# Kernel optimization log

Measured on AMD Instinct MI355X. Metric: run time of the kernel, lower is better.

## Reference

```python
import jax, jax.numpy as jnp
import numpy as np

BINS = 10


def _neg_pearson(p, t):
    # global standardization (torch.std default is unbiased, ddof=1)
    p = (p - p.mean()) / p.std(ddof=1)
    t = (t - t.mean()) / t.std(ddof=1)
    N = p.shape[1]
    sx = p.sum(1); sy = t.sum(1)
    sxy = (p * t).sum(1)
    sx2 = (p * p).sum(1); sy2 = (t * t).sum(1)
    pear = (N * sxy - sx * sy) / jnp.sqrt((N * sx2 - sx**2) * (N * sy2 - sy**2))
    return (1.0 - pear).mean()


def _hann(N):
    # torch.hann_window is periodic: 0.5*(1 - cos(2*pi*n/N))
    return 0.5 * (1.0 - jnp.cos(2.0 * jnp.pi * jnp.arange(N, dtype=jnp.float32) / N))


def _phase_correlation(x, t):
    # torch.stft with n_fft=seq_len, center=False, hann window -> single frame = rfft(x*hann)
    N = x.shape[1]
    w = _hann(N)
    xf = jnp.fft.rfft(x * w, axis=1)   # [B, N//2+1]
    tf = jnp.fft.rfft(t * w, axis=1)
    corr = xf * jnp.conj(tf)
    corr = corr / jnp.abs(corr)        # phase-only correlation
    cm = jnp.fft.irfft(corr, n=N, axis=1)  # [B, N]
    idx = jnp.argmax(cm, axis=1)
    return 1.0 - jnp.mean(jnp.cos(2.0 * jnp.pi * idx / N))


def _power_spectrum(x, t):
    xp = jnp.abs(jnp.fft.rfft(x, axis=1)) ** 2
    tp = jnp.abs(jnp.fft.rfft(t, axis=1)) ** 2
    return jnp.mean(jnp.abs(xp - tp)) / jnp.mean(tp)


def _mutual_information(x, y, bins=BINS):
    B, S = x.shape
    xmin = x.min(1); xmax = x.max(1)
    ymin = y.min(1); ymax = y.max(1)
    bwx = (xmax - xmin) / bins
    bwy = (ymax - ymin) / bins
    ix = jnp.clip(((x - xmin[:, None]) / bwx[:, None]).astype(jnp.int32), 0, bins - 1)
    iy = jnp.clip(((y - ymin[:, None]) / bwy[:, None]).astype(jnp.int32), 0, bins - 1)
    flat = ix * bins + iy  # [B, S]
    # vectorized 2D histogram via scatter-add (replaces the python double loop)
    hist = jax.vmap(lambda f: jnp.zeros(bins * bins, jnp.float32).at[f].add(1.0))(flat)
    hist = hist.reshape(B, bins, bins)
    hx = hist.sum(2); hy = hist.sum(1)
    denom = B * S  # NOTE: original normalizes by batch*seq (faithful reproduction)
    px = hx / denom; py = hy / denom; pxy = hist / denom
    eps = 1e-8
    mi = (pxy * jnp.log((pxy + eps) / (px[:, :, None] * py[:, None, :] + eps))).sum((1, 2))
    hxe = -(px * jnp.log(px + eps)).sum(1)
    hye = -(py * jnp.log(py + eps)).sum(1)
    nmi = mi / ((hxe + hye) / 2.0)
    return 1.0 - nmi.mean()


def setup_inputs() -> dict:
    key = jax.random.key(0)
    k1, k2 = jax.random.split(key)
    return {
        "predictions": jax.random.normal(k1, (2, 512, 16384), dtype=jnp.float32),
        "targets": jax.random.normal(k2, (512, 16384), dtype=jnp.float32),
        "i": 0,
        "epoch": 700,
    }


def reference(predictions, targets, i, epoch):
    p = predictions[i]  # [B, S]
    loss = _neg_pearson(p, targets)
    if epoch >= 400:
        loss = loss + _phase_correlation(p, targets)
        loss = loss + _power_spectrum(p, targets)
    if epoch >= 700:
        loss = loss + _mutual_information(p, targets)
    return loss
```

## Files before the change

kernel.cpp:

```cpp
#include <hip/hip_runtime.h>
#include <math.h>

#define BB 512
#define SS 16384
#define TPIF 6.28318530717958647692f

#define PD(i) ((i) + ((i) >> 4) + ((i) >> 8))
#define NPD 17472
#define BBASE 8200

__device__ __forceinline__ int sp(int k) {
    int s = ((k & 7) << 11) + (((k >> 3) & 7) << 8) + (((k >> 6) & 7) << 5)
          + (((k >> 9) & 7) << 2) + ((k >> 12) & 3);
    return PD(s);
}


template <int SGN, int LOG2Q>
__device__ __forceinline__ void stage_dif8(float2* sz, int t) {
    constexpr int Q = 1 << LOG2Q;
    constexpr int DQ = Q + (Q >> 4) + (Q >> 8);
    const float sg = (float)SGN;
    const float r2 = 0.70710678118654752f;
    #pragma unroll 1
    for (int c = 0; c < 2; ++c) {
        const int j = t + (c << 10);
        const int g = j >> LOG2Q;
        const int p = j & (Q - 1);
        const int i0 = PD((g << (LOG2Q + 3)) + p);
        int idx[8];
        #pragma unroll
        for (int k = 0; k < 8; ++k)
            idx[k] = (LOG2Q >= 4) ? (i0 + k * DQ) : (i0 + 4 * k + (k >> 2));
        float2 z[8];
        #pragma unroll
        for (int k = 0; k < 8; ++k) z[k] = sz[idx[k]];
        float2 a0, a1, a2, a3, b0, b1, b2, b3;
        a0 = make_float2(z[0].x + z[4].x, z[0].y + z[4].y);
        b0 = make_float2(z[0].x - z[4].x, z[0].y - z[4].y);
        a1 = make_float2(z[1].x + z[5].x, z[1].y + z[5].y);
        b1 = make_float2(z[1].x - z[5].x, z[1].y - z[5].y);
        a2 = make_float2(z[2].x + z[6].x, z[2].y + z[6].y);
        b2 = make_float2(z[2].x - z[6].x, z[2].y - z[6].y);
        a3 = make_float2(z[3].x + z[7].x, z[3].y + z[7].y);
        b3 = make_float2(z[3].x - z[7].x, z[3].y - z[7].y);
        { float x = b1.x, y = b1.y; b1 = make_float2(r2 * (x - sg * y), r2 * (y + sg * x)); }
        { float x = b2.x, y = b2.y; b2 = make_float2(-sg * y, sg * x); }
        { float x = b3.x, y = b3.y; b3 = make_float2(-r2 * (x + sg * y), r2 * (sg * x - y)); }
        float2 o[8];
        {
            float t0r = a0.x + a2.x, t0i = a0.y + a2.y;
            float t1r = a0.x - a2.x, t1i = a0.y - a2.y;
            float t2r = a1.x + a3.x, t2i = a1.y + a3.y;
            float t3r = a1.x - a3.x, t3i = a1.y - a3.y;
            o[0] = make_float2(t0r + t2r, t0i + t2i);
            o[4] = make_float2(t0r - t2r, t0i - t2i);
            o[2] = make_float2(t1r - sg * t3i, t1i + sg * t3r);
            o[6] = make_float2(t1r + sg * t3i, t1i - sg * t3r);
        }
        {
            float t0r = b0.x + b2.x, t0i = b0.y + b2.y;
            float t1r = b0.x - b2.x, t1i = b0.y - b2.y;
            float t2r = b1.x + b3.x, t2i = b1.y + b3.y;
            float t3r = b1.x - b3.x, t3i = b1.y - b3.y;
            o[1] = make_float2(t0r + t2r, t0i + t2i);
            o[5] = make_float2(t0r - t2r, t0i - t2i);
            o[3] = make_float2(t1r - sg * t3i, t1i + sg * t3r);
            o[7] = make_float2(t1r + sg * t3i, t1i - sg * t3r);
        }
        const float arev = sg * (float)p * (1.0f / (8.0f * (float)Q));
        const float cb = __builtin_amdgcn_cosf(arev);
        const float sb = __builtin_amdgcn_sinf(arev);
        sz[idx[0]] = o[0];
        float wr = cb, wi = sb;
        #pragma unroll
        for (int r = 1; r < 8; ++r) {
            sz[idx[r]] = make_float2(o[r].x * wr - o[r].y * wi,
                                     o[r].x * wi + o[r].y * wr);
            float nr = wr * cb - wi * sb, ni = wr * sb + wi * cb;
            wr = nr; wi = ni;
        }
    }
    __syncthreads();
}

template <int SGN>
__device__ __forceinline__ void stage_nt4(float2* sz, int t) {
    const float sg = (float)SGN;
    #pragma unroll 1
    for (int c = 0; c < 4; ++c) {
        const int j = t + (c << 10);
        const int i0 = 4 * j + (j >> 2) + (j >> 6);
        float2 z0 = sz[i0], z1 = sz[i0 + 1], z2 = sz[i0 + 2], z3 = sz[i0 + 3];
        float t0r = z0.x + z2.x, t0i = z0.y + z2.y;
        float t1r = z0.x - z2.x, t1i = z0.y - z2.y;
        float t2r = z1.x + z3.x, t2i = z1.y + z3.y;
        float t3r = z1.x - z3.x, t3i = z1.y - z3.y;
        sz[i0]     = make_float2(t0r + t2r, t0i + t2i);
        sz[i0 + 2] = make_float2(t0r - t2r, t0i - t2i);
        sz[i0 + 1] = make_float2(t1r - sg * t3i, t1i + sg * t3r);
        sz[i0 + 3] = make_float2(t1r + sg * t3i, t1i - sg * t3r);
    }
    __syncthreads();
}

template <int SGN, int LOG2Q>
__device__ __forceinline__ void stage8k_dif8(float2* bz, int t) {
    constexpr int Q = 1 << LOG2Q;
    constexpr int DQ = Q + (Q >> 4) + (Q >> 8);
    constexpr int CORR = (LOG2Q == 7) ? 1 : 0;
    const float sg = (float)SGN;
    const float r2 = 0.70710678118654752f;
    const int g = t >> LOG2Q;
    const int p = t & (Q - 1);
    const int i0 = PD((g << (LOG2Q + 3)) + p);
    int idx[8];
    #pragma unroll
    for (int k = 0; k < 8; ++k) idx[k] = i0 + k * DQ + CORR * (k >> 1);
    float2 z[8];
    #pragma unroll
    for (int k = 0; k < 8; ++k) z[k] = bz[idx[k]];
    float2 a0, a1, a2, a3, b0, b1, b2, b3;
    a0 = make_float2(z[0].x + z[4].x, z[0].y + z[4].y);
    b0 = make_float2(z[0].x - z[4].x, z[0].y - z[4].y);
    a1 = make_float2(z[1].x + z[5].x, z[1].y + z[5].y);
    b1 = make_float2(z[1].x - z[5].x, z[1].y - z[5].y);
    a2 = make_float2(z[2].x + z[6].x, z[2].y + z[6].y);
    b2 = make_float2(z[2].x - z[6].x, z[2].y - z[6].y);
    a3 = make_float2(z[3].x + z[7].x, z[3].y + z[7].y);
    b3 = make_float2(z[3].x - z[7].x, z[3].y - z[7].y);
    { float x = b1.x, y = b1.y; b1 = make_float2(r2 * (x - sg * y), r2 * (y + sg * x)); }
    { float x = b2.x, y = b2.y; b2 = make_float2(-sg * y, sg * x); }
    { float x = b3.x, y = b3.y; b3 = make_float2(-r2 * (x + sg * y), r2 * (sg * x - y)); }
    float2 o[8];
    {
        float t0r = a0.x + a2.x, t0i = a0.y + a2.y;
        float t1r = a0.x - a2.x, t1i = a0.y - a2.y;
        float t2r = a1.x + a3.x, t2i = a1.y + a3.y;
        float t3r = a1.x - a3.x, t3i = a1.y - a3.y;
        o[0] = make_float2(t0r + t2r, t0i + t2i);
        o[4] = make_float2(t0r - t2r, t0i - t2i);
        o[2] = make_float2(t1r - sg * t3i, t1i + sg * t3r);
        o[6] = make_float2(t1r + sg * t3i, t1i - sg * t3r);
    }
    {
        float t0r = b0.x + b2.x, t0i = b0.y + b2.y;
        float t1r = b0.x - b2.x, t1i = b0.y - b2.y;
        float t2r = b1.x + b3.x, t2i = b1.y + b3.y;
        float t3r = b1.x - b3.x, t3i = b1.y - b3.y;
        o[1] = make_float2(t0r + t2r, t0i + t2i);
        o[5] = make_float2(t0r - t2r, t0i - t2i);
        o[3] = make_float2(t1r - sg * t3i, t1i + sg * t3r);
        o[7] = make_float2(t1r + sg * t3i, t1i - sg * t3r);
    }
    const float arev = sg * (float)p * (1.0f / (8.0f * (float)Q));
    const float cb = __builtin_amdgcn_cosf(arev);
    const float sb = __builtin_amdgcn_sinf(arev);
    bz[idx[0]] = o[0];
    float wr = cb, wi = sb;
    #pragma unroll
    for (int r = 1; r < 8; ++r) {
        bz[idx[r]] = make_float2(o[r].x * wr - o[r].y * wi,
                                 o[r].x * wi + o[r].y * wr);
        float nr = wr * cb - wi * sb, ni = wr * sb + wi * cb;
        wr = nr; wi = ni;
    }
    __syncthreads();
}

template <int SGN>
__device__ __forceinline__ void stage8k_dif4(float2* bz, int t) {
    const float sg = (float)SGN;
    #pragma unroll 1
    for (int c = 0; c < 2; ++c) {
        const int j = t + (c << 10);
        const int g = j >> 2;
        const int p = j & 3;
        const int i0 = PD((g << 4) + p);
        float2 z0 = bz[i0], z1 = bz[i0 + 4], z2 = bz[i0 + 8], z3 = bz[i0 + 12];
        float t0r = z0.x + z2.x, t0i = z0.y + z2.y;
        float t1r = z0.x - z2.x, t1i = z0.y - z2.y;
        float t2r = z1.x + z3.x, t2i = z1.y + z3.y;
        float t3r = z1.x - z3.x, t3i = z1.y - z3.y;
        float b0r = t0r + t2r, b0i = t0i + t2i;
        float b2r = t0r - t2r, b2i = t0i - t2i;
        float b1r = t1r - sg * t3i, b1i = t1i + sg * t3r;
        float b3r = t1r + sg * t3i, b3i = t1i - sg * t3r;
        const float a = sg * (float)p * (1.0f / 16.0f);
        const float cb = __builtin_amdgcn_cosf(a);
        const float sb = __builtin_amdgcn_sinf(a);
        const float w2r = cb * cb - sb * sb, w2i = 2.0f * cb * sb;
        const float w3r = cb * w2r - sb * w2i, w3i = cb * w2i + sb * w2r;
        bz[i0]      = make_float2(b0r, b0i);
        bz[i0 + 4]  = make_float2(b1r * cb - b1i * sb,   b1r * sb + b1i * cb);
        bz[i0 + 8]  = make_float2(b2r * w2r - b2i * w2i, b2r * w2i + b2i * w2r);
        bz[i0 + 12] = make_float2(b3r * w3r - b3i * w3i, b3r * w3i + b3i * w3r);
    }
    __syncthreads();
}

template <int SGN>
__device__ __forceinline__ void stage8k_nt4(float2* bz, int t) {
    const float sg = (float)SGN;
    #pragma unroll 1
    for (int c = 0; c < 2; ++c) {
        const int j = t + (c << 10);
        const int i0 = 4 * j + (j >> 2) + (j >> 6);
        float2 z0 = bz[i0], z1 = bz[i0 + 1], z2 = bz[i0 + 2], z3 = bz[i0 + 3];
        float t0r = z0.x + z2.x, t0i = z0.y + z2.y;
        float t1r = z0.x - z2.x, t1i = z0.y - z2.y;
        float t2r = z1.x + z3.x, t2i = z1.y + z3.y;
        float t3r = z1.x - z3.x, t3i = z1.y - z3.y;
        bz[i0]     = make_float2(t0r + t2r, t0i + t2i);
        bz[i0 + 2] = make_float2(t0r - t2r, t0i - t2i);
        bz[i0 + 1] = make_float2(t1r - sg * t3i, t1i + sg * t3r);
        bz[i0 + 3] = make_float2(t1r + sg * t3i, t1i - sg * t3r);
    }
    __syncthreads();
}

__global__ __launch_bounds__(1024, 4) void k_main(const float* __restrict__ pred,
                                                  const float* __restrict__ targ,
                                                  const int* __restrict__ ip,
                                                  float* __restrict__ wpear,
                                                  float* __restrict__ wcos,
                                                  double* __restrict__ wnum,
                                                  double* __restrict__ wden,
                                                  float* __restrict__ wnmi) {
    __shared__ float2 sz[NPD];
    __shared__ double dpart[16 * 5];
    __shared__ float fpart[16 * 4];
    __shared__ int   subhist[400];
    __shared__ float hxm[10], hym[10];
    __shared__ float mterm[128];
    __shared__ float sbounds[4];
    __shared__ float svalw[16];
    __shared__ int   sidxw[16];

    const int row = blockIdx.x;
    const int t = threadIdx.x;
    const int w = t >> 6;
    const int lane = t & 63;
    float2* bz = &sz[BBASE];

    const float* xg = pred + (size_t)ip[0] * (size_t)BB * SS + (size_t)row * SS;
    const float* yg = targ + (size_t)row * SS;

    {
        const float4* xg4 = reinterpret_cast<const float4*>(xg);
        const float4* yg4 = reinterpret_cast<const float4*>(yg);
        double sx = 0, sy = 0, sxy = 0, sxx = 0, syy = 0;
        float xmn = 3.4e38f, xmx = -3.4e38f, ymn = 3.4e38f, ymx = -3.4e38f;
        #pragma unroll
        for (int m2 = 0; m2 < 4; ++m2) {
            int idx = t + (m2 << 10);
            float4 a = xg4[idx];
            float4 b = yg4[idx];
            int n0 = idx << 2;
            sz[PD(n0 + 0)] = make_float2(a.x, b.x);
            sz[PD(n0 + 1)] = make_float2(a.y, b.y);
            sz[PD(n0 + 2)] = make_float2(a.z, b.z);
            sz[PD(n0 + 3)] = make_float2(a.w, b.w);
            float av[4] = {a.x, a.y, a.z, a.w};
            float bv[4] = {b.x, b.y, b.z, b.w};
            #pragma unroll
            for (int c = 0; c < 4; ++c) {
                float aa = av[c], bb = bv[c];
                sx += (double)aa; sy += (double)bb;
                sxy += (double)aa * (double)bb;
                sxx += (double)aa * (double)aa;
                syy += (double)bb * (double)bb;
                xmn = fminf(xmn, aa); xmx = fmaxf(xmx, aa);
                ymn = fminf(ymn, bb); ymx = fmaxf(ymx, bb);
            }
        }
        #pragma unroll
        for (int o = 32; o > 0; o >>= 1) {
            sx += __shfl_down(sx, o, 64);  sy += __shfl_down(sy, o, 64);
            sxy += __shfl_down(sxy, o, 64);
            sxx += __shfl_down(sxx, o, 64); syy += __shfl_down(syy, o, 64);
            xmn = fminf(xmn, __shfl_down(xmn, o, 64));
            xmx = fmaxf(xmx, __shfl_down(xmx, o, 64));
            ymn = fminf(ymn, __shfl_down(ymn, o, 64));
            ymx = fmaxf(ymx, __shfl_down(ymx, o, 64));
        }
        if (lane == 0) {
            dpart[w*5+0] = sx; dpart[w*5+1] = sy; dpart[w*5+2] = sxy;
            dpart[w*5+3] = sxx; dpart[w*5+4] = syy;
            fpart[w*4+0] = xmn; fpart[w*4+1] = xmx; fpart[w*4+2] = ymn; fpart[w*4+3] = ymx;
        }
    }
    if (t < 400) subhist[t] = 0;
    __syncthreads();
    if (t == 0) {
        double v0=0,v1=0,v2=0,v3=0,v4=0;
        float b0=fpart[0], b1=fpart[1], b2=fpart[2], b3=fpart[3];
        for (int q = 0; q < 16; ++q) {
            v0 += dpart[q*5]; v1 += dpart[q*5+1]; v2 += dpart[q*5+2];
            v3 += dpart[q*5+3]; v4 += dpart[q*5+4];
            b0 = fminf(b0, fpart[q*4]);   b1 = fmaxf(b1, fpart[q*4+1]);
            b2 = fminf(b2, fpart[q*4+2]); b3 = fmaxf(b3, fpart[q*4+3]);
        }
        double N = (double)SS;
        double num = N * v2 - v0 * v1;
        double den = sqrt((N * v3 - v0 * v0) * (N * v4 - v1 * v1));
        wpear[row] = (float)(1.0 - num / den);
        sbounds[0] = b0; sbounds[1] = b1; sbounds[2] = b2; sbounds[3] = b3;
    }
    __syncthreads();

    {
        const float x0 = sbounds[0], bwx = (sbounds[1] - x0) / 10.0f;
        const float y0 = sbounds[2], bwy = (sbounds[3] - y0) / 10.0f;
        int* hsub = subhist + ((t >> 6) & 3) * 100;
        #pragma unroll 2
        for (int m = 0; m < 16; ++m) {
            float2 v = sz[PD(t + (m << 10))];
            int ix = (int)((v.x - x0) / bwx); ix = min(max(ix, 0), 9);
            int iy = (int)((v.y - y0) / bwy); iy = min(max(iy, 0), 9);
            atomicAdd(&hsub[ix * 10 + iy], 1);
        }
    }
    __syncthreads();
    if (t < 100) subhist[t] = subhist[t] + subhist[100+t] + subhist[200+t] + subhist[300+t];
    __syncthreads();
    if (t < 10) {
        int s1 = 0, s2 = 0;
        for (int j = 0; j < 10; ++j) { s1 += subhist[t*10+j]; s2 += subhist[j*10+t]; }
        hxm[t] = (float)s1; hym[t] = (float)s2;
    }
    __syncthreads();
    {
        float term = 0.0f;
        if (t < 100) {
            const float denom = 8388608.0f, eps = 1e-8f;
            float pxy = (float)subhist[t] / denom;
            float px = hxm[t / 10] / denom, py = hym[t % 10] / denom;
            term = pxy * logf((pxy + eps) / (px * py + eps));
        }
        if (t < 128) mterm[t] = (t < 100) ? term : 0.0f;
    }
    __syncthreads();
    if (t == 0) {
        const float denom = 8388608.0f, eps = 1e-8f;
        float mi = 0.0f;
        for (int q = 0; q < 100; ++q) mi += mterm[q];
        float hxe = 0.0f, hye = 0.0f;
        for (int q = 0; q < 10; ++q) {
            float px = hxm[q] / denom, py = hym[q] / denom;
            hxe -= px * logf(px + eps);
            hye -= py * logf(py + eps);
        }
        wnmi[row] = mi / (0.5f * (hxe + hye));
    }
    __syncthreads();

    stage_dif8<-1, 11>(sz, t);
    stage_dif8<-1,  8>(sz, t);
    stage_dif8<-1,  5>(sz, t);
    stage_dif8<-1,  2>(sz, t);
    stage_nt4<-1>(sz, t);

    {
        double anum = 0.0, aden = 0.0;
        float crv[8], civ[8];
        #pragma unroll 1
        for (int m = 0; m < 8; ++m) {
            int k = t + (m << 10);
            int km = (SS - k) & (SS - 1);
            float2 za = sz[sp(k)];
            float2 zb = sz[sp(km)];
            float ar  = za.x, ai  = za.y;
            float cr0 = zb.x, ci0 = zb.y;
            float xr = 0.5f * (ar + cr0), xi = 0.5f * (ai - ci0);
            float yr = 0.5f * (ai + ci0), yi = 0.5f * (cr0 - ar);
            float xp = xr * xr + xi * xi;
            float tp = yr * yr + yi * yi;
            anum += (double)fabsf(xp - tp);
            aden += (double)tp;
            float2 zap = sz[sp((k + 1) & (SS - 1))];
            float2 zam = sz[sp((k - 1) & (SS - 1))];
            float2 zbp = sz[sp((km + 1) & (SS - 1))];
            float2 zbm = sz[sp((km - 1) & (SS - 1))];
            float zwr = 0.5f * ar  - 0.25f * (zap.x + zam.x);
            float zwi = 0.5f * ai  - 0.25f * (zap.y + zam.y);
            float vwr = 0.5f * cr0 - 0.25f * (zbp.x + zbm.x);
            float vwi = 0.5f * ci0 - 0.25f * (zbp.y + zbm.y);
            float xwr = 0.5f * (zwr + vwr), xwi = 0.5f * (zwi - vwi);
            float ywr = 0.5f * (zwi + vwi), ywi = 0.5f * (vwr - zwr);
            float cr = xwr * ywr + xwi * ywi;
            float ci = xwi * ywr - xwr * ywi;
            float mag = sqrtf(cr * cr + ci * ci);
            crv[m] = cr / mag; civ[m] = ci / mag;
        }
        float c8 = 0.0f;
        if (t == 0) {
            float2 z0 = sz[sp(8192)];
            float2 zp = sz[sp(8193)];
            float2 zm = sz[sp(8191)];
            float ar = z0.x, ai = z0.y;
            anum += (double)fabsf(ar * ar - ai * ai);
            aden += (double)(ai * ai);
            float zwr = 0.5f * ar - 0.25f * (zp.x + zm.x);
            float zwi = 0.5f * ai - 0.25f * (zp.y + zm.y);
            float pr = zwr * zwi;
            c8 = pr / fabsf(pr);
        }
        #pragma unroll
        for (int o = 32; o > 0; o >>= 1) {
            anum += __shfl_down(anum, o, 64);
            aden += __shfl_down(aden, o, 64);
        }
        if (lane == 0) { dpart[w*2] = anum; dpart[w*2+1] = aden; }
        __syncthreads();
        #pragma unroll
        for (int m = 0; m < 8; ++m) {
            int k = t + (m << 10);
            sz[k] = make_float2(crv[m], civ[m]);
        }
        if (t == 0) {
            sz[8192] = make_float2(c8, 0.0f);
            double a = 0, b = 0;
            for (int q2_ = 0; q2_ < 16; ++q2_) { a += dpart[q2_*2]; b += dpart[q2_*2+1]; }
            wnum[row] = a; wden[row] = b;
        }
    }
    __syncthreads();

    {
        float a0 = (float)t * (1.0f / 16384.0f);
        float wr = __builtin_amdgcn_cosf(a0);
        float wi = __builtin_amdgcn_sinf(a0);
        const float cs = 0.92387953251128674f;
        const float sn = 0.38268343236508977f;
        const int pdt = PD(t);
        #pragma unroll 1
        for (int c = 0; c < 8; ++c) {
            int m = t + (c << 10);
            float2 cm = sz[m];
            float2 cn = sz[8192 - m];
            float Ax = cm.x + cn.x, Ay = cm.y - cn.y;
            float Dx = cm.x - cn.x, Dy = cm.y + cn.y;
            float WDx = Dx * wr - Dy * wi;
            float WDy = Dx * wi + Dy * wr;
            bz[pdt + c * 1092] = make_float2(Ax - WDy, Ay + WDx);
            float nr = wr * cs - wi * sn, ni = wr * sn + wi * cs;
            wr = nr; wi = ni;
        }
    }
    __syncthreads();

    stage8k_dif8<1, 10>(bz, t);
    stage8k_dif8<1,  7>(bz, t);
    stage8k_dif8<1,  4>(bz, t);
    stage8k_dif4<1>(bz, t);
    stage8k_nt4<1>(bz, t);

    {
        const int K = (((t >> 7) & 7) << 3) + (((t >> 4) & 7) << 6)
                    + (((t >> 2) & 3) << 9) + ((t & 3) << 11);
        const int pdt = PD(t);
        float bv = -3.4e38f; int bi = 0;
        #pragma unroll
        for (int c = 0; c < 8; ++c) {
            float2 z = bz[pdt + c * 1092];
            int n2 = (K + c) << 1;
            if (z.x > bv) { bv = z.x; bi = n2; }
            if (z.y > bv) { bv = z.y; bi = n2 + 1; }
        }
        #pragma unroll
        for (int o = 32; o > 0; o >>= 1) {
            float v2 = __shfl_down(bv, o, 64);
            int i2 = __shfl_down(bi, o, 64);
            if (v2 > bv || (v2 == bv && i2 < bi)) { bv = v2; bi = i2; }
        }
        if (lane == 0) { svalw[w] = bv; sidxw[w] = bi; }
    }
    __syncthreads();
    if (t == 0) {
        float bv = svalw[0]; int bi = sidxw[0];
        for (int q = 1; q < 16; ++q) {
            if (svalw[q] > bv || (svalw[q] == bv && sidxw[q] < bi)) { bv = svalw[q]; bi = sidxw[q]; }
        }
        wcos[row] = cosf(TPIF * (float)bi / 16384.0f);
    }
}

__global__ __launch_bounds__(512) void k_combine(const float* __restrict__ wpear,
                                                 const float* __restrict__ wcos,
                                                 const double* __restrict__ wnum,
                                                 const double* __restrict__ wden,
                                                 const float* __restrict__ wnmi,
                                                 const int* __restrict__ ep,
                                                 float* __restrict__ out) {
    __shared__ double dp[8 * 5];
    const int tid = threadIdx.x;
    const int w = tid >> 6, lane = tid & 63;
    double v0 = (double)wpear[tid], v1 = (double)wcos[tid];
    double v2 = wnum[tid], v3 = wden[tid], v4 = (double)wnmi[tid];
    #pragma unroll
    for (int o = 32; o > 0; o >>= 1) {
        v0 += __shfl_down(v0, o, 64); v1 += __shfl_down(v1, o, 64);
        v2 += __shfl_down(v2, o, 64); v3 += __shfl_down(v3, o, 64);
        v4 += __shfl_down(v4, o, 64);
    }
    if (lane == 0) {
        dp[w*5+0] = v0; dp[w*5+1] = v1; dp[w*5+2] = v2; dp[w*5+3] = v3; dp[w*5+4] = v4;
    }
    __syncthreads();
    if (tid == 0) {
        double s0=0,s1=0,s2=0,s3=0,s4=0;
        for (int q = 0; q < 8; ++q) {
            s0 += dp[q*5]; s1 += dp[q*5+1]; s2 += dp[q*5+2]; s3 += dp[q*5+3]; s4 += dp[q*5+4];
        }
        int epoch = ep[0];
        double loss = s0 / 512.0;
        if (epoch >= 400) {
            loss += 1.0 - s1 / 512.0;
            loss += s2 / s3;
        }
        if (epoch >= 700) {
            loss += 1.0 - s4 / 512.0;
        }
        out[0] = (float)loss;
    }
}

extern "C" void kernel_launch(void* const* d_in, const int* in_sizes, int n_in,
                              void* d_out, int out_size, void* d_ws, size_t ws_size,
                              hipStream_t stream) {
    const float* pred = (const float*)d_in[0];
    const float* targ = (const float*)d_in[1];
    const int* ip = (const int*)d_in[2];
    const int* ep = (const int*)d_in[3];
    float* out = (float*)d_out;

    double* wnum = (double*)d_ws;
    double* wden = wnum + BB;
    float* wpear = (float*)(wden + BB);
    float* wcos = wpear + BB;
    float* wnmi = wcos + BB;

    k_main<<<dim3(BB), dim3(1024), 0, stream>>>(pred, targ, ip, wpear, wcos, wnum, wden, wnmi);
    k_combine<<<dim3(1), dim3(512), 0, stream>>>(wpear, wcos, wnum, wden, wnmi, ep, out);
}
```

Baseline: 190.3 us.

## Fuse histogram into first FFT stage, merge inverse post-processing and argmax into stages

The mutual-information histogram is now built inside the first forward radix-8 FFT stage, reusing the values that stage already loads instead of making a separate shared-memory pass. Each wave gets its own sub-histogram to cut atomic contention. The inverse real-FFT post-processing is fused with the first inverse radix-8 stage, and the last radix-4 stage computes the argmax directly rather than writing back and rereading. The row moment sums move from double to float accumulation, which lowers precision for 16K-element sums and may shift the Pearson term slightly.

```diff
diff --git a/kernel.cpp b/kernel.cpp
--- a/kernel.cpp
+++ b/kernel.cpp
@@ -16,8 +16,11 @@
 }
 
 
-template <int SGN, int LOG2Q>
-__device__ __forceinline__ void stage_dif8(float2* sz, int t) {
+template <int SGN, int LOG2Q, bool DOMI = false>
+__device__ __forceinline__ void stage_dif8(float2* sz, int t,
+                                           float x0 = 0.f, float sbx = 0.f,
+                                           float y0 = 0.f, float sby = 0.f,
+                                           int* hsub = nullptr) {
     constexpr int Q = 1 << LOG2Q;
     constexpr int DQ = Q + (Q >> 4) + (Q >> 8);
     const float sg = (float)SGN;
@@ -35,6 +38,14 @@
         float2 z[8];
         #pragma unroll
         for (int k = 0; k < 8; ++k) z[k] = sz[idx[k]];
+        if constexpr (DOMI) {
+            #pragma unroll
+            for (int k = 0; k < 8; ++k) {
+                int ix = (int)((z[k].x - x0) * sbx); ix = min(max(ix, 0), 9);
+                int iy = (int)((z[k].y - y0) * sby); iy = min(max(iy, 0), 9);
+                atomicAdd(&hsub[ix * 10 + iy], 1);
+            }
+        }
         float2 a0, a1, a2, a3, b0, b1, b2, b3;
         a0 = make_float2(z[0].x + z[4].x, z[0].y + z[4].y);
         b0 = make_float2(z[0].x - z[4].x, z[0].y - z[4].y);
@@ -168,6 +179,79 @@
     __syncthreads();
 }
 
+__device__ __forceinline__ void inv_first(float2* sz, float2* bz, int t) {
+    const float r2 = 0.70710678118654752f;
+    float2 z[8];
+    {
+        float a0w = (float)t * (1.0f / 16384.0f);
+        float wr = __builtin_amdgcn_cosf(a0w);
+        float wi = __builtin_amdgcn_sinf(a0w);
+        const float cs = 0.92387953251128674f;
+        const float sn = 0.38268343236508977f;
+        #pragma unroll
+        for (int c = 0; c < 8; ++c) {
+            int m = t + (c << 10);
+            float2 cm = sz[m];
+            float2 cn = sz[8192 - m];
+            float Ax = cm.x + cn.x, Ay = cm.y - cn.y;
+            float Dx = cm.x - cn.x, Dy = cm.y + cn.y;
+            float WDx = Dx * wr - Dy * wi;
+            float WDy = Dx * wi + Dy * wr;
+            z[c] = make_float2(Ax - WDy, Ay + WDx);
+            float nr = wr * cs - wi * sn, ni = wr * sn + wi * cs;
+            wr = nr; wi = ni;
+        }
+    }
+    const float sg = 1.0f;
+    const int i0 = PD(t);
+    float2 a0, a1, a2, a3, b0, b1, b2, b3;
+    a0 = make_float2(z[0].x + z[4].x, z[0].y + z[4].y);
+    b0 = make_float2(z[0].x - z[4].x, z[0].y - z[4].y);
+    a1 = make_float2(z[1].x + z[5].x, z[1].y + z[5].y);
+    b1 = make_float2(z[1].x - z[5].x, z[1].y - z[5].y);
+    a2 = make_float2(z[2].x + z[6].x, z[2].y + z[6].y);
+    b2 = make_float2(z[2].x - z[6].x, z[2].y - z[6].y);
+    a3 = make_float2(z[3].x + z[7].x, z[3].y + z[7].y);
+    b3 = make_float2(z[3].x - z[7].x, z[3].y - z[7].y);
+    { float x = b1.x, y = b1.y; b1 = make_float2(r2 * (x - sg * y), r2 * (y + sg * x)); }
+    { float x = b2.x, y = b2.y; b2 = make_float2(-sg * y, sg * x); }
+    { float x = b3.x, y = b3.y; b3 = make_float2(-r2 * (x + sg * y), r2 * (sg * x - y)); }
+    float2 o[8];
+    {
+        float t0r = a0.x + a2.x, t0i = a0.y + a2.y;
+        float t1r = a0.x - a2.x, t1i = a0.y - a2.y;
+        float t2r = a1.x + a3.x, t2i = a1.y + a3.y;
+        float t3r = a1.x - a3.x, t3i = a1.y - a3.y;
+        o[0] = make_float2(t0r + t2r, t0i + t2i);
+        o[4] = make_float2(t0r - t2r, t0i - t2i);
+        o[2] = make_float2(t1r - sg * t3i, t1i + sg * t3r);
+        o[6] = make_float2(t1r + sg * t3i, t1i - sg * t3r);
+    }
+    {
+        float t0r = b0.x + b2.x, t0i = b0.y + b2.y;
+        float t1r = b0.x - b2.x, t1i = b0.y - b2.y;
+        float t2r = b1.x + b3.x, t2i = b1.y + b3.y;
+        float t3r = b1.x - b3.x, t3i = b1.y - b3.y;
+        o[1] = make_float2(t0r + t2r, t0i + t2i);
+        o[5] = make_float2(t0r - t2r, t0i - t2i);
+        o[3] = make_float2(t1r - sg * t3i, t1i + sg * t3r);
+        o[7] = make_float2(t1r + sg * t3i, t1i - sg * t3r);
+    }
+    const float arev = (float)t * (1.0f / 8192.0f);
+    const float cb = __builtin_amdgcn_cosf(arev);
+    const float sb = __builtin_amdgcn_sinf(arev);
+    bz[i0] = o[0];
+    float wr = cb, wi = sb;
+    #pragma unroll
+    for (int r = 1; r < 8; ++r) {
+        bz[i0 + r * 1092] = make_float2(o[r].x * wr - o[r].y * wi,
+                                        o[r].x * wi + o[r].y * wr);
+        float nr = wr * cb - wi * sb, ni = wr * sb + wi * cb;
+        wr = nr; wi = ni;
+    }
+    __syncthreads();
+}
+
 template <int SGN>
 __device__ __forceinline__ void stage8k_dif4(float2* bz, int t) {
     const float sg = (float)SGN;
@@ -199,9 +283,8 @@
     __syncthreads();
 }
 
-template <int SGN>
-__device__ __forceinline__ void stage8k_nt4(float2* bz, int t) {
-    const float sg = (float)SGN;
+__device__ __forceinline__ void inv_last_argmax(float2* bz, int t, float* pbv, int* pbi) {
+    float bv = -3.4e38f; int bi = 0;
     #pragma unroll 1
     for (int c = 0; c < 2; ++c) {
         const int j = t + (c << 10);
@@ -211,12 +294,20 @@
         float t1r = z0.x - z2.x, t1i = z0.y - z2.y;
         float t2r = z1.x + z3.x, t2i = z1.y + z3.y;
         float t3r = z1.x - z3.x, t3i = z1.y - z3.y;
-        bz[i0]     = make_float2(t0r + t2r, t0i + t2i);
-        bz[i0 + 2] = make_float2(t0r - t2r, t0i - t2i);
-        bz[i0 + 1] = make_float2(t1r - sg * t3i, t1i + sg * t3r);
-        bz[i0 + 3] = make_float2(t1r + sg * t3i, t1i - sg * t3r);
-    }
-    __syncthreads();
+        float re[4], im[4];
+        re[0] = t0r + t2r; im[0] = t0i + t2i;
+        re[1] = t1r - t3i; im[1] = t1i + t3r;
+        re[2] = t0r - t2r; im[2] = t0i - t2i;
+        re[3] = t1r + t3i; im[3] = t1i - t3r;
+        const int nb = (j >> 8) + ((j >> 5) & 7) * 8 + ((j >> 2) & 7) * 64 + (j & 3) * 512;
+        #pragma unroll
+        for (int k = 0; k < 4; ++k) {
+            int n2 = (nb + 2048 * k) << 1;
+            if (re[k] > bv || (re[k] == bv && n2 < bi)) { bv = re[k]; bi = n2; }
+            if (im[k] > bv || (im[k] == bv && n2 + 1 < bi)) { bv = im[k]; bi = n2 + 1; }
+        }
+    }
+    *pbv = bv; *pbi = bi;
 }
 
 __global__ __launch_bounds__(1024, 4) void k_main(const float* __restrict__ pred,
@@ -230,7 +321,7 @@
     __shared__ float2 sz[NPD];
     __shared__ double dpart[16 * 5];
     __shared__ float fpart[16 * 4];
-    __shared__ int   subhist[400];
+    __shared__ int   subhist[1600];
     __shared__ float hxm[10], hym[10];
     __shared__ float mterm[128];
     __shared__ float sbounds[4];
@@ -249,7 +340,7 @@
     {
         const float4* xg4 = reinterpret_cast<const float4*>(xg);
         const float4* yg4 = reinterpret_cast<const float4*>(yg);
-        double sx = 0, sy = 0, sxy = 0, sxx = 0, syy = 0;
+        float sx = 0, sy = 0, sxy = 0, sxx = 0, syy = 0;
         float xmn = 3.4e38f, xmx = -3.4e38f, ymn = 3.4e38f, ymx = -3.4e38f;
         #pragma unroll
         for (int m2 = 0; m2 < 4; ++m2) {
@@ -266,10 +357,10 @@
             #pragma unroll
             for (int c = 0; c < 4; ++c) {
                 float aa = av[c], bb = bv[c];
-                sx += (double)aa; sy += (double)bb;
-                sxy += (double)aa * (double)bb;
-                sxx += (double)aa * (double)aa;
-                syy += (double)bb * (double)bb;
+                sx += aa; sy += bb;
+                sxy += aa * bb;
+                sxx += aa * aa;
+                syy += bb * bb;
                 xmn = fminf(xmn, aa); xmx = fmaxf(xmx, aa);
                 ymn = fminf(ymn, bb); ymx = fmaxf(ymx, bb);
             }
@@ -285,12 +376,14 @@
             ymx = fmaxf(ymx, __shfl_down(ymx, o, 64));
         }
         if (lane == 0) {
-            dpart[w*5+0] = sx; dpart[w*5+1] = sy; dpart[w*5+2] = sxy;
-            dpart[w*5+3] = sxx; dpart[w*5+4] = syy;
+            dpart[w*5+0] = (double)sx; dpart[w*5+1] = (double)sy;
+            dpart[w*5+2] = (double)sxy;
+            dpart[w*5+3] = (double)sxx; dpart[w*5+4] = (double)syy;
             fpart[w*4+0] = xmn; fpart[w*4+1] = xmx; fpart[w*4+2] = ymn; fpart[w*4+3] = ymx;
         }
     }
-    if (t < 400) subhist[t] = 0;
+    subhist[t] = 0;
+    if (t < 576) subhist[1024 + t] = 0;
     __syncthreads();
     if (t == 0) {
         double v0=0,v1=0,v2=0,v3=0,v4=0;
@@ -305,24 +398,24 @@
         double num = N * v2 - v0 * v1;
         double den = sqrt((N * v3 - v0 * v0) * (N * v4 - v1 * v1));
         wpear[row] = (float)(1.0 - num / den);
-        sbounds[0] = b0; sbounds[1] = b1; sbounds[2] = b2; sbounds[3] = b3;
-    }
-    __syncthreads();
-
-    {
-        const float x0 = sbounds[0], bwx = (sbounds[1] - x0) / 10.0f;
-        const float y0 = sbounds[2], bwy = (sbounds[3] - y0) / 10.0f;
-        int* hsub = subhist + ((t >> 6) & 3) * 100;
-        #pragma unroll 2
-        for (int m = 0; m < 16; ++m) {
-            float2 v = sz[PD(t + (m << 10))];
-            int ix = (int)((v.x - x0) / bwx); ix = min(max(ix, 0), 9);
-            int iy = (int)((v.y - y0) / bwy); iy = min(max(iy, 0), 9);
-            atomicAdd(&hsub[ix * 10 + iy], 1);
-        }
-    }
-    __syncthreads();
-    if (t < 100) subhist[t] = subhist[t] + subhist[100+t] + subhist[200+t] + subhist[300+t];
+        sbounds[0] = b0; sbounds[1] = 10.0f / (b1 - b0);
+        sbounds[2] = b2; sbounds[3] = 10.0f / (b3 - b2);
+    }
+    __syncthreads();
+
+    {
+        const float x0 = sbounds[0], sbx = sbounds[1];
+        const float y0 = sbounds[2], sby = sbounds[3];
+        int* hsub = subhist + w * 100;
+        stage_dif8<-1, 11, true>(sz, t, x0, sbx, y0, sby, hsub);
+    }
+
+    if (t < 100) {
+        int s = 0;
+        #pragma unroll
+        for (int q = 0; q < 16; ++q) s += subhist[t + 100 * q];
+        subhist[t] = s;
+    }
     __syncthreads();
     if (t < 10) {
         int s1 = 0, s2 = 0;
@@ -353,9 +446,7 @@
         }
         wnmi[row] = mi / (0.5f * (hxe + hye));
     }
-    __syncthreads();
-
-    stage_dif8<-1, 11>(sz, t);
+
     stage_dif8<-1,  8>(sz, t);
     stage_dif8<-1,  5>(sz, t);
     stage_dif8<-1,  2>(sz, t);
@@ -427,47 +518,13 @@
     }
     __syncthreads();
 
-    {
-        float a0 = (float)t * (1.0f / 16384.0f);
-        float wr = __builtin_amdgcn_cosf(a0);
-        float wi = __builtin_amdgcn_sinf(a0);
-        const float cs = 0.92387953251128674f;
-        const float sn = 0.38268343236508977f;
-        const int pdt = PD(t);
-        #pragma unroll 1
-        for (int c = 0; c < 8; ++c) {
-            int m = t + (c << 10);
-            float2 cm = sz[m];
-            float2 cn = sz[8192 - m];
-            float Ax = cm.x + cn.x, Ay = cm.y - cn.y;
-            float Dx = cm.x - cn.x, Dy = cm.y + cn.y;
-            float WDx = Dx * wr - Dy * wi;
-            float WDy = Dx * wi + Dy * wr;
-            bz[pdt + c * 1092] = make_float2(Ax - WDy, Ay + WDx);
-            float nr = wr * cs - wi * sn, ni = wr * sn + wi * cs;
-            wr = nr; wi = ni;
-        }
-    }
-    __syncthreads();
-
-    stage8k_dif8<1, 10>(bz, t);
+    inv_first(sz, bz, t);
     stage8k_dif8<1,  7>(bz, t);
     stage8k_dif8<1,  4>(bz, t);
     stage8k_dif4<1>(bz, t);
-    stage8k_nt4<1>(bz, t);
-
-    {
-        const int K = (((t >> 7) & 7) << 3) + (((t >> 4) & 7) << 6)
-                    + (((t >> 2) & 3) << 9) + ((t & 3) << 11);
-        const int pdt = PD(t);
-        float bv = -3.4e38f; int bi = 0;
-        #pragma unroll
-        for (int c = 0; c < 8; ++c) {
-            float2 z = bz[pdt + c * 1092];
-            int n2 = (K + c) << 1;
-            if (z.x > bv) { bv = z.x; bi = n2; }
-            if (z.y > bv) { bv = z.y; bi = n2 + 1; }
-        }
+    {
+        float bv; int bi;
+        inv_last_argmax(bz, t, &bv, &bi);
         #pragma unroll
         for (int o = 32; o > 0; o >>= 1) {
             float v2 = __shfl_down(bv, o, 64);
```

Measured after the change: 180.2 us. 1.06x faster.
